# Kernel tuning notes

Hardware: AMD Instinct MI355X
Metric: run time of the kernel (lower is better)

The kernel has to match this reference:

```python
import jax, jax.numpy as jnp
from jax import lax
import numpy as np


def setup_inputs() -> dict:
    key = jax.random.key(0)
    k1, k2 = jax.random.split(key)
    sat_features = jax.random.normal(k1, (128, 4, 64, 16), dtype=jnp.float32)  # [B_s, h, w, c]
    grd_features = jax.random.normal(k2, (128, 4, 64, 16), dtype=jnp.float32)  # [B_g, h, gw, c]
    return {"sat_features": sat_features, "grd_features": grd_features}


def reference(sat_features, grd_features):
    B_s, h, w, c = sat_features.shape
    B_g, gh, gw, gc = grd_features.shape
    assert h == gh and c == gc

    # --- corr: circular cross-correlation over width via conv2d ---
    n = gw - 1
    sat_pad = jnp.concatenate([sat_features, sat_features[:, :, :n, :]], axis=2)  # [B_s,h,w+n,c]
    rhs = jnp.transpose(grd_features, (1, 2, 3, 0))  # HWIO: [h,gw,c,B_g]
    out = lax.conv_general_dilated(
        sat_pad, rhs, window_strides=(1, 1), padding='VALID',
        dimension_numbers=('NHWC', 'HWIO', 'NHWC'))  # [B_s,1,w,B_g]
    corr = out[:, 0, :, :]                  # [B_s, w, B_g]
    orien = jnp.argmax(corr, axis=1)        # [B_s, B_g] int

    # --- crop_sat: circular-shift gather along width, crop to grd width ---
    shift = orien % w                                                   # [B_s,B_g]
    idx = (jnp.arange(gw)[None, None, :] + shift[:, :, None]) % w       # [B_s,B_g,gw]
    # gather: sat_crop[i,j,y,k,ch] = sat_features[i, y, idx[i,j,k], ch]
    sat_crop = jnp.take_along_axis(
        sat_features[:, None],              # [B_s,1,h,w,c]
        idx[:, :, None, :, None],           # [B_s,B_g,1,gw,1]
        axis=3)                             # -> [B_s,B_g,h,gw,c]

    # --- L2 normalize per (sat,grd) pair and squared-chord distance ---
    norm = jnp.sqrt(jnp.sum(sat_crop * sat_crop, axis=(2, 3, 4), keepdims=True))
    sat_matrix = sat_crop / jnp.maximum(norm, 1e-12)
    dot = jnp.sum(sat_matrix * grd_features[None], axis=(2, 3, 4))      # [B_s,B_g]
    distance = 2.0 - 2.0 * dot.T                                        # [B_g,B_s]

    return sat_features, grd_features, distance, orien
```

## Files before the change

### kernel.cpp

```cpp
#include <hip/hip_runtime.h>
#include <math.h>

typedef _Float16 f16;
typedef __attribute__((ext_vector_type(8))) _Float16 f16x8;
typedef __attribute__((ext_vector_type(16))) float f32x16;

#define DIST_OFF  1048576
#define ORI_OFF   1064960
#define SATP_STR  72

#define MFMA(a,b,c) __builtin_amdgcn_mfma_f32_32x32x16_f16((a),(b),(c),0,0,0)

__global__ __launch_bounds__(256) void prep_k(const float* __restrict__ grd,
                                              f16* __restrict__ gHi, f16* __restrict__ gLo,
                                              const float4* __restrict__ satIn,
                                              const float4* __restrict__ grdIn,
                                              float4* __restrict__ out4) {
    const int b = blockIdx.x;
    if (b >= 64) {
        int i = (b - 64) * 256 + threadIdx.x;
        out4[i] = satIn[i];
        out4[131072 + i] = grdIn[i];
        return;
    }
    __shared__ f16 tH[8192], tL[8192];
    const int tid = threadIdx.x;
    const int g0 = (b & 7) * 16;
    const int kq = b >> 3;
    #pragma unroll
    for (int i = 0; i < 32; ++i) {
        int flat = i * 256 + tid;
        int g_l = flat >> 9;
        int r   = flat & 511;
        int h   = r >> 7;
        int j   = r & 127;
        float v = grd[(((g0 + g_l) * 4 + h) * 64 + kq * 8) * 16 + j];
        int k_l = (j >> 4) * 64 + h * 16 + (j & 15);
        f16 hv = (f16)v;
        int a = (k_l >> 3) * 128 + g_l * 8 + (k_l & 7);
        tH[a] = hv;
        tL[a] = (f16)(v - (float)hv);
    }
    __syncthreads();
    #pragma unroll
    for (int i = 0; i < 4; ++i) {
        int f = i * 256 + tid;
        int dst = (kq * 64 + (f >> 4)) * 128 + g0 + (f & 15);
        ((f16x8*)gHi)[dst] = *(const f16x8*)(tH + f * 8);
        ((f16x8*)gLo)[dst] = *(const f16x8*)(tL + f * 8);
    }
}

__global__ __launch_bounds__(512, 2) void corr_k(const float* __restrict__ sat,
                                                 const f16* __restrict__ gHi,
                                                 const f16* __restrict__ gLo,
                                                 float* __restrict__ out) {
    __shared__ __align__(16) unsigned char smem[131072];
    __shared__ float wred[8];
    __shared__ float rnormS;
    f16* sH = (f16*)smem;
    f16* sL = sH + 127 * SATP_STR;
    float* red = (float*)smem;

    const int tid = threadIdx.x;
    const int s  = blockIdx.x >> 1;
    const int gh = blockIdx.x & 1;
    const int wave = tid >> 6, lane = tid & 63;
    const int m = lane & 31, half = lane >> 5;

    const float* satS = sat + s * 4096;
    float ssq = 0.f;
    #pragma unroll
    for (int r = 0; r < 8; ++r) {
        int idx = r * 512 + tid;
        float v = satS[idx];
        int h = idx >> 10, w = (idx >> 4) & 63, c = idx & 15;
        int col = h * 16 + c;
        f16 hv = (f16)v, lv = (f16)(v - (float)hv);
        sH[w * SATP_STR + col] = hv;
        sL[w * SATP_STR + col] = lv;
        if (w < 63) { sH[(w + 64) * SATP_STR + col] = hv; sL[(w + 64) * SATP_STR + col] = lv; }
        ssq += v * v;
    }
    #pragma unroll
    for (int off = 32; off > 0; off >>= 1) ssq += __shfl_down(ssq, off, 64);
    if (lane == 0) wred[wave] = ssq;
    __syncthreads();
    if (tid == 0) {
        float t = 0.f;
        #pragma unroll
        for (int i = 0; i < 8; ++i) t += wred[i];
        rnormS = 1.f / fmaxf(sqrtf(t), 1e-12f);
    }

    const f16* A0h = sH + m * SATP_STR + half * 8;
    const f16* A0l = sL + m * SATP_STR + half * 8;
    const f16x8* BHp = (const f16x8*)gHi;
    const f16x8* BLp = (const f16x8*)gLo;
    const int ggBase = half * 128 + gh * 64 + m;

    f32x16 z;
    #pragma unroll
    for (int r = 0; r < 16; ++r) z[r] = 0.f;
    f32x16 h00 = z, h01 = z, h10 = z, h11 = z, x00 = z, x01 = z, x10 = z, x11 = z;

    f16x8 ah[2][2], al[2][2], bh[2][2], bl[2][2];

#define LOADT(p, t) { \
    int tc = (t) > 255 ? 255 : (t); \
    int ao = (tc >> 2) * SATP_STR + (tc & 3) * 16; \
    ah[p][0] = *(const f16x8*)(A0h + ao); \
    ah[p][1] = *(const f16x8*)(A0h + ao + 32 * SATP_STR); \
    al[p][0] = *(const f16x8*)(A0l + ao); \
    al[p][1] = *(const f16x8*)(A0l + ao + 32 * SATP_STR); \
    int bu = tc * 256 + ggBase; \
    bh[p][0] = BHp[bu]; bh[p][1] = BHp[bu + 32]; \
    bl[p][0] = BLp[bu]; bl[p][1] = BLp[bu + 32]; }

#define STEP(p) { \
    h00 = MFMA(ah[p][0], bh[p][0], h00); \
    h01 = MFMA(ah[p][0], bh[p][1], h01); \
    h10 = MFMA(ah[p][1], bh[p][0], h10); \
    h11 = MFMA(ah[p][1], bh[p][1], h11); \
    x00 = MFMA(ah[p][0], bl[p][0], x00); x00 = MFMA(al[p][0], bh[p][0], x00); \
    x01 = MFMA(ah[p][0], bl[p][1], x01); x01 = MFMA(al[p][0], bh[p][1], x01); \
    x10 = MFMA(ah[p][1], bl[p][0], x10); x10 = MFMA(al[p][1], bh[p][0], x10); \
    x11 = MFMA(ah[p][1], bl[p][1], x11); x11 = MFMA(al[p][1], bh[p][1], x11); }

    const int t0 = wave * 32;
    LOADT(0, t0)
    #pragma unroll 4
    for (int t = t0; t < t0 + 32; t += 2) {
        LOADT(1, t + 1)
        STEP(0)
        LOADT(0, t + 2)
        STEP(1)
    }
    h00 = h00 + x00; h01 = h01 + x01; h10 = h10 + x10; h11 = h11 + x11;

    __syncthreads();
    float* rw = red + wave * 4096;
    #pragma unroll
    for (int r = 0; r < 16; ++r) {
        int j0 = (r & 3) + 8 * (r >> 2) + 4 * half;
        rw[j0 * 64 + m]             = h00[r];
        rw[j0 * 64 + 32 + m]        = h01[r];
        rw[(j0 + 32) * 64 + m]      = h10[r];
        rw[(j0 + 32) * 64 + 32 + m] = h11[r];
    }
    __syncthreads();
    #pragma unroll
    for (int i = 0; i < 8; ++i) {
        int c = i * 512 + tid;
        float v = red[c]         + red[c + 4096]  + red[c + 8192]  + red[c + 12288]
                + red[c + 16384] + red[c + 20480] + red[c + 24576] + red[c + 28672];
        red[c] = v;
    }
    __syncthreads();

    if (tid < 64) {
        int g = tid;
        float best = red[g];
        int bj = 0;
        for (int j = 1; j < 64; ++j) {
            float v = red[j * 64 + g];
            if (v > best) { best = v; bj = j; }
        }
        float dot = best * rnormS;
        int gg = gh * 64 + g;
        out[DIST_OFF + gg * 128 + s] = 2.f - 2.f * dot;
        out[ORI_OFF + s * 128 + gg]  = (float)bj;
    }
}

__global__ void copy_k(const float4* __restrict__ a, const float4* __restrict__ b,
                       float4* __restrict__ out) {
    int i = blockIdx.x * 256 + threadIdx.x;
    out[i] = a[i];
    out[131072 + i] = b[i];
}

extern "C" void kernel_launch(void* const* d_in, const int* in_sizes, int n_in,
                              void* d_out, int out_size, void* d_ws, size_t ws_size,
                              hipStream_t stream) {
    const float* sat = (const float*)d_in[0];
    const float* grd = (const float*)d_in[1];
    float* out = (float*)d_out;

    const bool useWs = false;
    f16* gHi;
    f16* gLo;
    if (useWs) {
        gHi = (f16*)d_ws;
        gLo = gHi + 524288;
    } else {
        gHi = (f16*)out;
        gLo = (f16*)(out + 262144);
    }

    prep_k<<<useWs ? 576 : 64, 256, 0, stream>>>(grd, gHi, gLo,
                                                 (const float4*)sat, (const float4*)grd,
                                                 (float4*)out);
    corr_k<<<256, 512, 0, stream>>>(sat, gHi, gLo, out);
    if (!useWs)
        copy_k<<<512, 256, 0, stream>>>((const float4*)sat, (const float4*)grd, (float4*)out);
}
```

Before: 88.95 us.

## Fuse grd conversion, output copy and argmax into single corr kernel

Removes the separate prep kernel that pre-split grd into fp16 hi/lo tiles and the trailing copy kernel. The corr kernel now loads fp32 grd directly from global memory and converts it to hi/lo fp16 inside the MFMA loop. It also performs the input passthrough copy itself and runs the argmax over width in two parallel stages instead of a serial 64-step loop on one wave. This cuts two kernel launches and an intermediate buffer round-trip. In exchange, every block reads fp32 grd (twice the bytes, strided per lane) and repeats the conversion work redundantly.

```diff
diff --git a/kernel.cpp b/kernel.cpp
--- a/kernel.cpp
+++ b/kernel.cpp
@@ -11,53 +11,29 @@
 
 #define MFMA(a,b,c) __builtin_amdgcn_mfma_f32_32x32x16_f16((a),(b),(c),0,0,0)
 
-__global__ __launch_bounds__(256) void prep_k(const float* __restrict__ grd,
-                                              f16* __restrict__ gHi, f16* __restrict__ gLo,
-                                              const float4* __restrict__ satIn,
-                                              const float4* __restrict__ grdIn,
-                                              float4* __restrict__ out4) {
-    const int b = blockIdx.x;
-    if (b >= 64) {
-        int i = (b - 64) * 256 + threadIdx.x;
-        out4[i] = satIn[i];
-        out4[131072 + i] = grdIn[i];
-        return;
+__device__ inline void cvt8(float4 a, float4 b, f16x8* hi, f16x8* lo) {
+    float va[8] = {a.x, a.y, a.z, a.w, b.x, b.y, b.z, b.w};
+    f16x8 h, l;
+    #pragma unroll
+    for (int e = 0; e < 8; ++e) {
+        f16 hv = (f16)va[e];
+        h[e] = hv;
+        l[e] = (f16)(va[e] - (float)hv);
     }
-    __shared__ f16 tH[8192], tL[8192];
-    const int tid = threadIdx.x;
-    const int g0 = (b & 7) * 16;
-    const int kq = b >> 3;
-    #pragma unroll
-    for (int i = 0; i < 32; ++i) {
-        int flat = i * 256 + tid;
-        int g_l = flat >> 9;
-        int r   = flat & 511;
-        int h   = r >> 7;
-        int j   = r & 127;
-        float v = grd[(((g0 + g_l) * 4 + h) * 64 + kq * 8) * 16 + j];
-        int k_l = (j >> 4) * 64 + h * 16 + (j & 15);
-        f16 hv = (f16)v;
-        int a = (k_l >> 3) * 128 + g_l * 8 + (k_l & 7);
-        tH[a] = hv;
-        tL[a] = (f16)(v - (float)hv);
-    }
-    __syncthreads();
-    #pragma unroll
-    for (int i = 0; i < 4; ++i) {
-        int f = i * 256 + tid;
-        int dst = (kq * 64 + (f >> 4)) * 128 + g0 + (f & 15);
-        ((f16x8*)gHi)[dst] = *(const f16x8*)(tH + f * 8);
-        ((f16x8*)gLo)[dst] = *(const f16x8*)(tL + f * 8);
-    }
+    *hi = h; *lo = l;
 }
 
 __global__ __launch_bounds__(512, 2) void corr_k(const float* __restrict__ sat,
-                                                 const f16* __restrict__ gHi,
-                                                 const f16* __restrict__ gLo,
-                                                 float* __restrict__ out) {
+                                                 const float* __restrict__ grd,
+                                                 float* __restrict__ out,
+                                                 const float4* __restrict__ satIn,
+                                                 const float4* __restrict__ grdIn,
+                                                 float4* __restrict__ out4) {
     __shared__ __align__(16) unsigned char smem[131072];
     __shared__ float wred[8];
     __shared__ float rnormS;
+    __shared__ float pBest[512];
+    __shared__ int   pIdx[512];
     f16* sH = (f16*)smem;
     f16* sL = sH + 127 * SATP_STR;
     float* red = (float*)smem;
@@ -95,9 +71,8 @@
 
     const f16* A0h = sH + m * SATP_STR + half * 8;
     const f16* A0l = sL + m * SATP_STR + half * 8;
-    const f16x8* BHp = (const f16x8*)gHi;
-    const f16x8* BLp = (const f16x8*)gLo;
-    const int ggBase = half * 128 + gh * 64 + m;
+    const float* BgA = grd + (gh * 64 + m) * 4096 + half * 8;
+    const float* BgB = BgA + 32 * 4096;
 
     f32x16 z;
     #pragma unroll
@@ -106,16 +81,23 @@
 
     f16x8 ah[2][2], al[2][2], bh[2][2], bl[2][2];
 
-#define LOADT(p, t) { \
+#define LOADA(p, t) { \
     int tc = (t) > 255 ? 255 : (t); \
     int ao = (tc >> 2) * SATP_STR + (tc & 3) * 16; \
     ah[p][0] = *(const f16x8*)(A0h + ao); \
     ah[p][1] = *(const f16x8*)(A0h + ao + 32 * SATP_STR); \
     al[p][0] = *(const f16x8*)(A0l + ao); \
-    al[p][1] = *(const f16x8*)(A0l + ao + 32 * SATP_STR); \
-    int bu = tc * 256 + ggBase; \
-    bh[p][0] = BHp[bu]; bh[p][1] = BHp[bu + 32]; \
-    bl[p][0] = BLp[bu]; bl[p][1] = BLp[bu + 32]; }
+    al[p][1] = *(const f16x8*)(A0l + ao + 32 * SATP_STR); }
+
+#define LOADB(p, t) { \
+    int tc = (t) > 255 ? 255 : (t); \
+    int fo = (tc & 3) * 1024 + (tc >> 2) * 16; \
+    float4 u0 = *(const float4*)(BgA + fo); \
+    float4 u1 = *(const float4*)(BgA + fo + 4); \
+    float4 w0 = *(const float4*)(BgB + fo); \
+    float4 w1 = *(const float4*)(BgB + fo + 4); \
+    cvt8(u0, u1, &bh[p][0], &bl[p][0]); \
+    cvt8(w0, w1, &bh[p][1], &bl[p][1]); }
 
 #define STEP(p) { \
     h00 = MFMA(ah[p][0], bh[p][0], h00); \
@@ -128,12 +110,12 @@
     x11 = MFMA(ah[p][1], bl[p][1], x11); x11 = MFMA(al[p][1], bh[p][1], x11); }
 
     const int t0 = wave * 32;
-    LOADT(0, t0)
+    LOADA(0, t0) LOADB(0, t0)
     #pragma unroll 4
     for (int t = t0; t < t0 + 32; t += 2) {
-        LOADT(1, t + 1)
+        LOADA(1, t + 1) LOADB(1, t + 1)
         STEP(0)
-        LOADT(0, t + 2)
+        LOADA(0, t + 2) LOADB(0, t + 2)
         STEP(1)
     }
     h00 = h00 + x00; h01 = h01 + x01; h10 = h10 + x10; h11 = h11 + x11;
@@ -158,26 +140,38 @@
     }
     __syncthreads();
 
+    {
+        int g = tid & 63, jq = tid >> 6;
+        int jb = jq * 8;
+        float best = red[jb * 64 + g];
+        int bj = jb;
+        #pragma unroll
+        for (int jj = 1; jj < 8; ++jj) {
+            float v = red[(jb + jj) * 64 + g];
+            if (v > best) { best = v; bj = jb + jj; }
+        }
+        pBest[tid] = best; pIdx[tid] = bj;
+    }
+    __syncthreads();
     if (tid < 64) {
         int g = tid;
-        float best = red[g];
-        int bj = 0;
-        for (int j = 1; j < 64; ++j) {
-            float v = red[j * 64 + g];
-            if (v > best) { best = v; bj = j; }
+        float best = pBest[g]; int bj = pIdx[g];
+        #pragma unroll
+        for (int jq = 1; jq < 8; ++jq) {
+            float v = pBest[jq * 64 + g];
+            if (v > best) { best = v; bj = pIdx[jq * 64 + g]; }
         }
         float dot = best * rnormS;
         int gg = gh * 64 + g;
         out[DIST_OFF + gg * 128 + s] = 2.f - 2.f * dot;
         out[ORI_OFF + s * 128 + gg]  = (float)bj;
     }
-}
 
-__global__ void copy_k(const float4* __restrict__ a, const float4* __restrict__ b,
-                       float4* __restrict__ out) {
-    int i = blockIdx.x * 256 + threadIdx.x;
-    out[i] = a[i];
-    out[131072 + i] = b[i];
+    {
+        int i = blockIdx.x * 512 + tid;
+        out4[i] = satIn[i];
+        out4[131072 + i] = grdIn[i];
+    }
 }
 
 extern "C" void kernel_launch(void* const* d_in, const int* in_sizes, int n_in,
@@ -186,22 +180,6 @@
     const float* sat = (const float*)d_in[0];
     const float* grd = (const float*)d_in[1];
     float* out = (float*)d_out;
-
-    const bool useWs = false;
-    f16* gHi;
-    f16* gLo;
-    if (useWs) {
-        gHi = (f16*)d_ws;
-        gLo = gHi + 524288;
-    } else {
-        gHi = (f16*)out;
-        gLo = (f16*)(out + 262144);
-    }
-
-    prep_k<<<useWs ? 576 : 64, 256, 0, stream>>>(grd, gHi, gLo,
-                                                 (const float4*)sat, (const float4*)grd,
-                                                 (float4*)out);
-    corr_k<<<256, 512, 0, stream>>>(sat, gHi, gLo, out);
-    if (!useWs)
-        copy_k<<<512, 256, 0, stream>>>((const float4*)sat, (const float4*)grd, (float4*)out);
+    corr_k<<<256, 512, 0, stream>>>(sat, grd, out,
+                                    (const float4*)sat, (const float4*)grd, (float4*)out);
 }
```

After: 92.04 us. 1.03x slower.
